# Kernel optimization log

Hardware: AMD Instinct MI355X
Metric: run time of the kernel (lower is better)

Reference implementation:

```python
import jax, jax.numpy as jnp
import numpy as np

N_DRUG = 572
EMB = 256
K_NB = 128
N_TAIL = 100000
N_REL = 200
N_EDGE = 4576
BN_EPS = 1e-5


def setup_inputs() -> dict:
    key = jax.random.key(0)
    ks = jax.random.split(key, 12)
    return {
        "drug_name": jnp.arange(N_DRUG, dtype=jnp.int64 if jax.config.jax_enable_x64 else jnp.int32),
        "adj_tail": jax.random.randint(ks[0], (N_DRUG, K_NB), 0, N_TAIL),
        "adj_relation": jax.random.randint(ks[1], (N_DRUG, K_NB), 0, N_REL),
        "nb_src": jax.random.randint(ks[2], (N_EDGE,), 0, N_DRUG),
        "nb_dst": jax.random.randint(ks[3], (N_EDGE,), 0, N_DRUG),
        "epoch": 2,
        # learned parameters
        "drug_table": jax.random.normal(ks[4], (N_DRUG, EMB), dtype=jnp.float32),
        "rela_table": jax.random.normal(ks[5], (N_REL, EMB), dtype=jnp.float32),
        "ent_table": jax.random.normal(ks[6], (N_TAIL, EMB), dtype=jnp.float32),
        "lin_W": jax.random.normal(ks[7], (2 * EMB, EMB), dtype=jnp.float32) * (1.0 / np.sqrt(2 * EMB)),
        "lin_b": jnp.zeros((EMB,), dtype=jnp.float32),
        "bn_gamma": jnp.ones((EMB,), dtype=jnp.float32),
        "bn_beta": jnp.zeros((EMB,), dtype=jnp.float32),
    }


def reference(drug_name, adj_tail, adj_relation, nb_src, nb_dst, epoch,
              drug_table, rela_table, ent_table, lin_W, lin_b, bn_gamma, bn_beta):
    # --- embedding gathers ---
    d = drug_table[drug_name]          # [N, E]
    r = rela_table[adj_relation]       # [N, K, E]
    e = ent_table[adj_tail]            # [N, K, E]

    # --- attention over sampled neighbors (KGNN-style: score = <drug, relation>) ---
    scores = jnp.einsum('ne,nke->nk', d, r)              # [N, K]
    alpha = jax.nn.softmax(scores, axis=1)               # softmax over neighbors
    attended = jnp.einsum('nk,nke->ne', alpha, e)        # [N, E]

    # --- Linear(2E -> E) + ReLU + BatchNorm1d (training-mode batch stats) ---
    x = jnp.concatenate([attended, d], axis=1)           # [N, 2E]
    h = jax.nn.relu(x @ lin_W + lin_b)                   # [N, E]
    mean = jnp.mean(h, axis=0)
    var = jnp.mean((h - mean) ** 2, axis=0)              # biased var, as in torch BN
    drug_f = (h - mean) * jax.lax.rsqrt(var + BN_EPS) * bn_gamma + bn_beta

    # --- invariant-adjacency segment-average scatter update (epoch > 1) ---
    if epoch > 1:
        nb_sum = jax.ops.segment_sum(drug_f[nb_src], nb_dst, num_segments=N_DRUG)   # [N, E]
        cnt = jax.ops.segment_sum(jnp.ones_like(nb_dst, dtype=drug_f.dtype), nb_dst,
                                  num_segments=N_DRUG)                               # [N]
        nb_avg = nb_sum / jnp.maximum(cnt, 1.0)[:, None]
        drug_f = jnp.where((cnt > 0)[:, None], (nb_avg + drug_f) * 0.5, drug_f)
    return drug_f
```

## Files before the change

kernel.cpp:

```cpp
#include <hip/hip_runtime.h>

#define N_DRUG 572
#define EMB    256
#define K_NB   128
#define N_EDGE 4576
#define BN_EPS 1e-5f
#define NCHUNK 4

__global__ __launch_bounds__(256) void scores2_kernel(
    const int* __restrict__ drug_name,
    const int* __restrict__ adj_relation,
    const float* __restrict__ drug_table,
    const float* __restrict__ rela_table,
    float* __restrict__ scores)
{
    const int b    = blockIdx.x / NCHUNK;
    const int c    = blockIdx.x % NCHUNK;
    const int tid  = threadIdx.x;
    const int lane = tid & 63;
    const int wv   = tid >> 6;

    const float4 dv =
        ((const float4*)(drug_table + (size_t)drug_name[b] * EMB))[lane];

    const int kbase = c * 32 + wv * 8;
    float p[8];
    #pragma unroll
    for (int j = 0; j < 8; ++j) {
        const int rel = adj_relation[b * K_NB + kbase + j];
        const float4 rv =
            ((const float4*)(rela_table + (size_t)rel * EMB))[lane];
        p[j] = dv.x * rv.x + dv.y * rv.y + dv.z * rv.z + dv.w * rv.w;
    }
    #pragma unroll
    for (int j = 0; j < 8; ++j) {
        float s = p[j];
        #pragma unroll
        for (int off = 32; off > 0; off >>= 1)
            s += __shfl_xor(s, off, 64);
        if (lane == 0) scores[(size_t)b * K_NB + kbase + j] = s;
    }
}

__global__ __launch_bounds__(256) void gather2_kernel(
    const int* __restrict__ adj_tail,
    const float* __restrict__ scores,
    const float* __restrict__ ent_table,
    float* __restrict__ att)
{
    __shared__ float sc[K_NB];
    __shared__ float wred[2];
    __shared__ float part[4][EMB];

    const int b    = blockIdx.x / NCHUNK;
    const int c    = blockIdx.x % NCHUNK;
    const int tid  = threadIdx.x;
    const int lane = tid & 63;
    const int wv   = tid >> 6;

    if (tid < K_NB) sc[tid] = scores[(size_t)b * K_NB + tid];
    __syncthreads();

    float pv = 0.f;
    if (tid < K_NB) {
        float m = sc[tid];
        #pragma unroll
        for (int off = 32; off > 0; off >>= 1)
            m = fmaxf(m, __shfl_xor(m, off, 64));
        if (lane == 0) wred[wv] = m;
    }
    __syncthreads();
    if (tid < K_NB) {
        const float m = fmaxf(wred[0], wred[1]);
        pv = __expf(sc[tid] - m);
        float s = pv;
        #pragma unroll
        for (int off = 32; off > 0; off >>= 1)
            s += __shfl_xor(s, off, 64);
        if (lane == 0) wred[wv] = s;
    }
    __syncthreads();
    if (tid < K_NB) sc[tid] = pv / (wred[0] + wred[1]);
    __syncthreads();

    const int kbase = c * 32 + wv * 8;
    float4 acc = make_float4(0.f, 0.f, 0.f, 0.f);
    #pragma unroll
    for (int j = 0; j < 8; ++j) {
        const int k = kbase + j;
        const float a = sc[k];
        const int   t = adj_tail[b * K_NB + k];
        const float4 ev = ((const float4*)(ent_table + (size_t)t * EMB))[lane];
        acc.x = fmaf(a, ev.x, acc.x);
        acc.y = fmaf(a, ev.y, acc.y);
        acc.z = fmaf(a, ev.z, acc.z);
        acc.w = fmaf(a, ev.w, acc.w);
    }
    ((float4*)part[wv])[lane] = acc;
    __syncthreads();
    const float v = part[0][tid] + part[1][tid] + part[2][tid] + part[3][tid];
    atomicAdd(&att[(size_t)b * EMB + tid], v);
}

__global__ __launch_bounds__(512) void linear_kernel(
    const int* __restrict__ drug_name,
    const float* __restrict__ att,
    const float* __restrict__ drug_table,
    const float* __restrict__ lin_W,
    const float* __restrict__ lin_b,
    float* __restrict__ h,
    float* __restrict__ s1,
    float* __restrict__ s2)
{
    __shared__ float xs[2 * EMB];
    __shared__ float part[2][EMB];

    const int b   = blockIdx.x;
    const int tid = threadIdx.x;

    if (tid < EMB) xs[tid] = att[(size_t)b * EMB + tid];
    else           xs[tid] = drug_table[(size_t)drug_name[b] * EMB + (tid - EMB)];
    __syncthreads();

    const int col  = tid & (EMB - 1);
    const int half = tid >> 8;
    const float* wp = lin_W + (size_t)(half * EMB) * EMB + col;
    const float* xp = xs + half * EMB;
    float acc = 0.f;
    #pragma unroll 16
    for (int i = 0; i < EMB; ++i)
        acc = fmaf(xp[i], wp[(size_t)i * EMB], acc);
    part[half][col] = acc;
    __syncthreads();

    if (tid < EMB) {
        const float v = fmaxf(part[0][tid] + part[1][tid] + lin_b[tid], 0.f);
        h[(size_t)b * EMB + tid] = v;
        atomicAdd(&s1[tid], v);
        atomicAdd(&s2[tid], v * v);
    }
}

#define EPB 2
__global__ __launch_bounds__(256) void scatter_bn(
    const int* __restrict__ nb_src, const int* __restrict__ nb_dst,
    const int* __restrict__ epoch,
    const float* __restrict__ h,
    const float* __restrict__ s1, const float* __restrict__ s2,
    const float* __restrict__ gamma, const float* __restrict__ beta,
    float* __restrict__ nb_sum,
    float* __restrict__ cnt)
{
    if (*epoch <= 1) return;
    const int tid = threadIdx.x;
    const float invN  = 1.0f / (float)N_DRUG;
    const float mean  = s1[tid] * invN;
    const float var   = s2[tid] * invN - mean * mean;
    const float scale = gamma[tid] * rsqrtf(var + BN_EPS);
    const float bet   = beta[tid];

    const int e0 = blockIdx.x * EPB;
    #pragma unroll
    for (int e = e0; e < e0 + EPB; ++e) {
        const int s = nb_src[e];
        const int d = nb_dst[e];
        const float f = (h[(size_t)s * EMB + tid] - mean) * scale + bet;
        atomicAdd(&nb_sum[(size_t)d * EMB + tid], f);
        if (tid == 0) atomicAdd(&cnt[d], 1.0f);
    }
}

__global__ __launch_bounds__(256) void combine_bn(
    const float* __restrict__ h,
    const float* __restrict__ s1, const float* __restrict__ s2,
    const float* __restrict__ gamma, const float* __restrict__ beta,
    const float* __restrict__ nb_sum,
    const float* __restrict__ cnt,
    const int* __restrict__ epoch,
    float* __restrict__ out)
{
    const int b   = blockIdx.x;
    const int tid = threadIdx.x;
    const size_t idx = (size_t)b * EMB + tid;
    const float invN  = 1.0f / (float)N_DRUG;
    const float mean  = s1[tid] * invN;
    const float var   = s2[tid] * invN - mean * mean;
    const float scale = gamma[tid] * rsqrtf(var + BN_EPS);
    float f = (h[idx] - mean) * scale + beta[tid];
    if (*epoch > 1) {
        const float c = cnt[b];
        if (c > 0.f) f = (nb_sum[idx] / c + f) * 0.5f;
    }
    out[idx] = f;
}

extern "C" void kernel_launch(void* const* d_in, const int* in_sizes, int n_in,
                              void* d_out, int out_size, void* d_ws, size_t ws_size,
                              hipStream_t stream) {
    const int*   drug_name    = (const int*)d_in[0];
    const int*   adj_tail     = (const int*)d_in[1];
    const int*   adj_relation = (const int*)d_in[2];
    const int*   nb_src       = (const int*)d_in[3];
    const int*   nb_dst       = (const int*)d_in[4];
    const int*   epoch        = (const int*)d_in[5];
    const float* drug_table   = (const float*)d_in[6];
    const float* rela_table   = (const float*)d_in[7];
    const float* ent_table    = (const float*)d_in[8];
    const float* lin_W        = (const float*)d_in[9];
    const float* lin_b        = (const float*)d_in[10];
    const float* bn_gamma     = (const float*)d_in[11];
    const float* bn_beta      = (const float*)d_in[12];
    float* out = (float*)d_out;

    float* ws = (float*)d_ws;
    float* h      = ws;
    float* s1     = h + N_DRUG * EMB;
    float* s2     = s1 + EMB;
    float* cnt    = s2 + EMB;
    float* nb_sum = cnt + N_DRUG;
    float* att    = nb_sum + N_DRUG * EMB;
    float* scores = att + N_DRUG * EMB;
    const size_t zero_bytes =
        (size_t)(EMB + EMB + N_DRUG + 2 * N_DRUG * EMB) * sizeof(float);

    hipMemsetAsync(s1, 0, zero_bytes, stream);

    scores2_kernel<<<N_DRUG * NCHUNK, 256, 0, stream>>>(drug_name, adj_relation,
                                                        drug_table, rela_table, scores);

    gather2_kernel<<<N_DRUG * NCHUNK, 256, 0, stream>>>(adj_tail, scores,
                                                        ent_table, att);

    linear_kernel<<<N_DRUG, 512, 0, stream>>>(drug_name, att, drug_table,
                                              lin_W, lin_b, h, s1, s2);

    scatter_bn<<<N_EDGE / EPB, 256, 0, stream>>>(nb_src, nb_dst, epoch,
                                                 h, s1, s2, bn_gamma, bn_beta,
                                                 nb_sum, cnt);

    combine_bn<<<N_DRUG, 256, 0, stream>>>(h, s1, s2, bn_gamma, bn_beta,
                                           nb_sum, cnt, epoch, out);
}
```

Baseline: 220.9 us.

## Fuse score and gather kernels; write per-chunk partials instead of atomics

Merges the relation-score kernel into the softmax/gather kernel. Each of the 4 chunk blocks per drug now recomputes all 128 scores itself, which removes one launch and the scores round-trip through global memory. In exchange, rela_table reads are duplicated 4x. The atomicAdd into att is replaced by plain per-chunk partial writes that linear_kernel sums, which also shrinks the memset.

```diff
diff --git a/kernel.cpp b/kernel.cpp
--- a/kernel.cpp
+++ b/kernel.cpp
@@ -5,17 +5,22 @@
 #define K_NB   128
 #define N_EDGE 4576
 #define BN_EPS 1e-5f
-#define NCHUNK 4
-
-__global__ __launch_bounds__(256) void scores2_kernel(
+
+__global__ __launch_bounds__(256) void sg_kernel(
     const int* __restrict__ drug_name,
+    const int* __restrict__ adj_tail,
     const int* __restrict__ adj_relation,
     const float* __restrict__ drug_table,
     const float* __restrict__ rela_table,
-    float* __restrict__ scores)
-{
-    const int b    = blockIdx.x / NCHUNK;
-    const int c    = blockIdx.x % NCHUNK;
+    const float* __restrict__ ent_table,
+    float* __restrict__ att4)
+{
+    __shared__ float sc[K_NB];
+    __shared__ float wred[2];
+    __shared__ float part[4][EMB];
+
+    const int b    = blockIdx.x >> 2;
+    const int c    = blockIdx.x & 3;
     const int tid  = threadIdx.x;
     const int lane = tid & 63;
     const int wv   = tid >> 6;
@@ -23,71 +28,54 @@
     const float4 dv =
         ((const float4*)(drug_table + (size_t)drug_name[b] * EMB))[lane];
 
-    const int kbase = c * 32 + wv * 8;
-    float p[8];
     #pragma unroll
-    for (int j = 0; j < 8; ++j) {
-        const int rel = adj_relation[b * K_NB + kbase + j];
-        const float4 rv =
-            ((const float4*)(rela_table + (size_t)rel * EMB))[lane];
-        p[j] = dv.x * rv.x + dv.y * rv.y + dv.z * rv.z + dv.w * rv.w;
-    }
-    #pragma unroll
-    for (int j = 0; j < 8; ++j) {
-        float s = p[j];
-        #pragma unroll
-        for (int off = 32; off > 0; off >>= 1)
-            s += __shfl_xor(s, off, 64);
-        if (lane == 0) scores[(size_t)b * K_NB + kbase + j] = s;
-    }
-}
-
-__global__ __launch_bounds__(256) void gather2_kernel(
-    const int* __restrict__ adj_tail,
-    const float* __restrict__ scores,
-    const float* __restrict__ ent_table,
-    float* __restrict__ att)
-{
-    __shared__ float sc[K_NB];
-    __shared__ float wred[2];
-    __shared__ float part[4][EMB];
-
-    const int b    = blockIdx.x / NCHUNK;
-    const int c    = blockIdx.x % NCHUNK;
-    const int tid  = threadIdx.x;
-    const int lane = tid & 63;
-    const int wv   = tid >> 6;
-
-    if (tid < K_NB) sc[tid] = scores[(size_t)b * K_NB + tid];
+    for (int batch = 0; batch < 4; ++batch) {
+        const int kb = wv * 32 + batch * 8;
+        float p[8];
+        #pragma unroll
+        for (int j = 0; j < 8; ++j) {
+            const int rel = adj_relation[b * K_NB + kb + j];
+            const float4 rv =
+                ((const float4*)(rela_table + (size_t)rel * EMB))[lane];
+            p[j] = dv.x * rv.x + dv.y * rv.y + dv.z * rv.z + dv.w * rv.w;
+        }
+        #pragma unroll
+        for (int j = 0; j < 8; ++j) {
+            float s = p[j];
+            #pragma unroll
+            for (int off = 32; off; off >>= 1) s += __shfl_xor(s, off, 64);
+            if (lane == 0) sc[kb + j] = s;
+        }
+    }
     __syncthreads();
 
     float pv = 0.f;
     if (tid < K_NB) {
         float m = sc[tid];
         #pragma unroll
-        for (int off = 32; off > 0; off >>= 1)
+        for (int off = 32; off; off >>= 1)
             m = fmaxf(m, __shfl_xor(m, off, 64));
         if (lane == 0) wred[wv] = m;
     }
     __syncthreads();
+    const float gmax = fmaxf(wred[0], wred[1]);
+    __syncthreads();
     if (tid < K_NB) {
-        const float m = fmaxf(wred[0], wred[1]);
-        pv = __expf(sc[tid] - m);
+        pv = __expf(sc[tid] - gmax);
         float s = pv;
         #pragma unroll
-        for (int off = 32; off > 0; off >>= 1)
-            s += __shfl_xor(s, off, 64);
+        for (int off = 32; off; off >>= 1) s += __shfl_xor(s, off, 64);
         if (lane == 0) wred[wv] = s;
     }
     __syncthreads();
     if (tid < K_NB) sc[tid] = pv / (wred[0] + wred[1]);
     __syncthreads();
 
-    const int kbase = c * 32 + wv * 8;
+    const int kb2 = c * 32 + wv * 8;
     float4 acc = make_float4(0.f, 0.f, 0.f, 0.f);
     #pragma unroll
     for (int j = 0; j < 8; ++j) {
-        const int k = kbase + j;
+        const int k = kb2 + j;
         const float a = sc[k];
         const int   t = adj_tail[b * K_NB + k];
         const float4 ev = ((const float4*)(ent_table + (size_t)t * EMB))[lane];
@@ -98,13 +86,13 @@
     }
     ((float4*)part[wv])[lane] = acc;
     __syncthreads();
-    const float v = part[0][tid] + part[1][tid] + part[2][tid] + part[3][tid];
-    atomicAdd(&att[(size_t)b * EMB + tid], v);
+    att4[(size_t)blockIdx.x * EMB + tid] =
+        part[0][tid] + part[1][tid] + part[2][tid] + part[3][tid];
 }
 
 __global__ __launch_bounds__(512) void linear_kernel(
     const int* __restrict__ drug_name,
-    const float* __restrict__ att,
+    const float* __restrict__ att4,
     const float* __restrict__ drug_table,
     const float* __restrict__ lin_W,
     const float* __restrict__ lin_b,
@@ -118,8 +106,12 @@
     const int b   = blockIdx.x;
     const int tid = threadIdx.x;
 
-    if (tid < EMB) xs[tid] = att[(size_t)b * EMB + tid];
-    else           xs[tid] = drug_table[(size_t)drug_name[b] * EMB + (tid - EMB)];
+    if (tid < EMB) {
+        const float* a0 = att4 + (size_t)(b * 4) * EMB;
+        xs[tid] = a0[tid] + a0[EMB + tid] + a0[2 * EMB + tid] + a0[3 * EMB + tid];
+    } else {
+        xs[tid] = drug_table[(size_t)drug_name[b] * EMB + (tid - EMB)];
+    }
     __syncthreads();
 
     const int col  = tid & (EMB - 1);
@@ -218,20 +210,17 @@
     float* s2     = s1 + EMB;
     float* cnt    = s2 + EMB;
     float* nb_sum = cnt + N_DRUG;
-    float* att    = nb_sum + N_DRUG * EMB;
-    float* scores = att + N_DRUG * EMB;
+    float* att4   = nb_sum + N_DRUG * EMB;
     const size_t zero_bytes =
-        (size_t)(EMB + EMB + N_DRUG + 2 * N_DRUG * EMB) * sizeof(float);
+        (size_t)(EMB + EMB + N_DRUG + N_DRUG * EMB) * sizeof(float);
 
     hipMemsetAsync(s1, 0, zero_bytes, stream);
 
-    scores2_kernel<<<N_DRUG * NCHUNK, 256, 0, stream>>>(drug_name, adj_relation,
-                                                        drug_table, rela_table, scores);
-
-    gather2_kernel<<<N_DRUG * NCHUNK, 256, 0, stream>>>(adj_tail, scores,
-                                                        ent_table, att);
-
-    linear_kernel<<<N_DRUG, 512, 0, stream>>>(drug_name, att, drug_table,
+    sg_kernel<<<N_DRUG * 4, 256, 0, stream>>>(drug_name, adj_tail, adj_relation,
+                                              drug_table, rela_table, ent_table,
+                                              att4);
+
+    linear_kernel<<<N_DRUG, 512, 0, stream>>>(drug_name, att4, drug_table,
                                               lin_W, lin_b, h, s1, s2);
 
     scatter_bn<<<N_EDGE / EPB, 256, 0, stream>>>(nb_src, nb_dst, epoch,
```

Measured after the change: 230.8 us. 4.5% more time.
